# Optimization experiments

Hardware: AMD Instinct MI355X
Metric: run time of the kernel (lower is better)

Reference implementation:

```python
import jax, jax.numpy as jnp
import numpy as np

N_ENTITY = 64368
N_REL = 40
DIM = 128
N_BASES = 8
N_EDGES = 500000
BATCH = 64
SEED_LEN = 32


def _glorot(k, shape, gain=1.414):
    fan_in, fan_out = shape[0], shape[1]
    bound = gain * np.sqrt(6.0 / (fan_in + fan_out))
    return jax.random.uniform(k, shape, jnp.float32, -bound, bound)


def setup_inputs() -> dict:
    key = jax.random.key(0)
    ks = jax.random.split(key, 11)
    return dict(
        seed_ids=jax.random.randint(ks[0], (BATCH, SEED_LEN), 0, N_ENTITY),
        edge_src=jax.random.randint(ks[1], (N_EDGES,), 0, N_ENTITY),
        edge_dst=jax.random.randint(ks[2], (N_EDGES,), 0, N_ENTITY),
        edge_type=jax.random.randint(ks[3], (N_EDGES,), 0, N_REL),
        basis=jax.random.normal(ks[4], (N_BASES, N_ENTITY, DIM), jnp.float32) * 0.02,
        att=jax.random.normal(ks[5], (N_REL, N_BASES), jnp.float32) * 0.1,
        root=jax.random.normal(ks[6], (N_ENTITY, DIM), jnp.float32) * 0.02,
        rgcn_bias=jnp.zeros((DIM,), jnp.float32),
        attn_a=_glorot(ks[7], (DIM, DIM)),
        attn_b=_glorot(ks[8], (DIM, 1)),
        out_bias=jnp.zeros((N_ENTITY,), jnp.float32),
    )


def _rgcn_nodes(basis, att, root, rgcn_bias, edge_src, edge_dst, edge_type):
    # RGCNConv with x=None: message for edge e is row src[e] of w[type[e]],
    # where w = att @ basis (basis decomposition); 'mean' aggregation to dst;
    # update: aggr + root + bias.
    n_entity, dim = root.shape
    coeff = att[edge_type]  # [E, nb]
    agg = jnp.zeros((n_entity, dim), jnp.float32)
    for b in range(basis.shape[0]):  # small fixed loop over bases
        m = basis[b][edge_src] * coeff[:, b][:, None]  # [E, dim]
        agg = agg + jax.ops.segment_sum(m, edge_dst, num_segments=n_entity)
    deg = jax.ops.segment_sum(jnp.ones_like(edge_dst, jnp.float32), edge_dst,
                              num_segments=n_entity)
    agg = agg / jnp.maximum(deg, 1.0)[:, None]
    return agg + root + rgcn_bias[None, :]


def reference(seed_ids, edge_src, edge_dst, edge_type, basis, att, root,
              rgcn_bias, attn_a, attn_b, out_bias):
    nodes = _rgcn_nodes(basis, att, root, rgcn_bias, edge_src, edge_dst, edge_type)
    # self-attention pooling over each seed set (all entries valid / non-empty)
    H = nodes[seed_ids]  # [B, S, D]
    e = jnp.einsum('bsd,d->bs', jnp.tanh(jnp.einsum('bsd,de->bse', H, attn_a)),
                   attn_b[:, 0])  # [B, S]
    attn = jax.nn.softmax(e, axis=-1)
    u = jnp.einsum('bs,bsd->bd', attn, H)  # [B, D]
    # scores = F.linear(u, nodes_features, output.bias)
    scores = u @ nodes.T + out_bias[None, :]  # [B, n_entity]
    return scores
```

## Files before the change

### kernel.cpp

```cpp
#include <hip/hip_runtime.h>
#include <hip/hip_fp16.h>

#define N_ENTITY 64368
#define N_REL 40
#define DIM 128
#define N_BASES 8
#define N_EDGES 500000
#define BATCH 64
#define SEED_LEN 32
#define NROWS (BATCH * SEED_LEN)
#define SCAN_NB ((N_ENTITY + 255) / 256)
#define NPAD (SCAN_NB * 256)

#define CAP 64
#define OVF_CAP 4096
#define SCAT4_BLOCKS ((N_EDGES / 4 + 255) / 256)
#define CVT_BLOCKS 2048


struct alignas(16) h8 { __half2 a, b, c, d; };

__device__ __forceinline__ void scat1(
    int s, int d, int y, int* __restrict__ cnt, int* __restrict__ novf,
    int* __restrict__ ovf, int* __restrict__ slots)
{
    int meta = s * 64 + y;
    int k = atomicAdd(&cnt[d], 1);
    if (k < CAP) {
        slots[(size_t)d * CAP + k] = meta;
    } else {
        int o = atomicAdd(novf, 1);
        if (o < OVF_CAP) { ovf[2 * o] = d; ovf[2 * o + 1] = meta; }
    }
}

__global__ __launch_bounds__(256) void k_prep(
    const int* __restrict__ esrc, const int* __restrict__ edst,
    const int* __restrict__ etype, const float* __restrict__ basis,
    __half* __restrict__ basis16, int* __restrict__ cnt,
    int* __restrict__ novf, int* __restrict__ ovf, int* __restrict__ slots)
{
    int bid = blockIdx.x, tid = threadIdx.x;
    if (bid < SCAT4_BLOCKS) {
        int e4 = (bid * 256 + tid) * 4;
        if (e4 < N_EDGES) {
            int4 s4 = *(const int4*)(esrc + e4);
            int4 d4 = *(const int4*)(edst + e4);
            int4 y4 = *(const int4*)(etype + e4);
            scat1(s4.x, d4.x, y4.x, cnt, novf, ovf, slots);
            scat1(s4.y, d4.y, y4.y, cnt, novf, ovf, slots);
            scat1(s4.z, d4.z, y4.z, cnt, novf, ovf, slots);
            scat1(s4.w, d4.w, y4.w, cnt, novf, ovf, slots);
        }
    } else {
        int lane = tid & 63;
        int l32  = lane & 31;
        int hw   = lane >> 5;
        int wv   = ((bid - SCAT4_BLOCKS) << 2) + (tid >> 6);
        const size_t bstride = (size_t)N_ENTITY * DIM;

        for (int e2 = wv; 2 * e2 < N_ENTITY; e2 += (CVT_BLOCKS << 2)) {
            int e = 2 * e2 + hw;
            if (e >= N_ENTITY) continue;
            const float* sp = basis + (size_t)e * DIM + (l32 << 2);
            __half* dp = basis16 + ((size_t)e << 10) + (l32 << 5);
            #pragma unroll
            for (int it = 0; it < 4; ++it) {
                float4 v0 = *(const float4*)(sp + (size_t)(2 * it)     * bstride);
                float4 v1 = *(const float4*)(sp + (size_t)(2 * it + 1) * bstride);
                h8 o;
                o.a = __floats2half2_rn(v0.x, v0.y);
                o.b = __floats2half2_rn(v0.z, v0.w);
                o.c = __floats2half2_rn(v1.x, v1.y);
                o.d = __floats2half2_rn(v1.z, v1.w);
                *(h8*)(dp + it * 8) = o;
            }
        }
    }
}

__device__ __forceinline__ void acc_edge2(
    const h8& q0, const h8& q1, float4 c, float4& acc)
{
    float2 f;
    f = __half22float2(q0.a); acc.x += c.x * f.x; acc.y += c.x * f.y;
    f = __half22float2(q0.b); acc.z += c.x * f.x; acc.w += c.x * f.y;
    f = __half22float2(q0.c); acc.x += c.y * f.x; acc.y += c.y * f.y;
    f = __half22float2(q0.d); acc.z += c.y * f.x; acc.w += c.y * f.y;
    f = __half22float2(q1.a); acc.x += c.z * f.x; acc.y += c.z * f.y;
    f = __half22float2(q1.b); acc.z += c.z * f.x; acc.w += c.z * f.y;
    f = __half22float2(q1.c); acc.x += c.w * f.x; acc.y += c.w * f.y;
    f = __half22float2(q1.d); acc.z += c.w * f.x; acc.w += c.w * f.y;
}

__global__ __launch_bounds__(256) void k_gather16(
    const int* __restrict__ cnt, const int* __restrict__ novf,
    const int* __restrict__ ovf, const int* __restrict__ slots,
    const __half* __restrict__ basis16, const float* __restrict__ att,
    const float* __restrict__ root, const float* __restrict__ bias,
    float* __restrict__ agg)
{
    __shared__ float att_s[N_REL * N_BASES];
    int tid = threadIdx.x;
    for (int i = tid; i < N_REL * N_BASES; i += 256) att_s[i] = att[i];
    __syncthreads();

    int wid  = (int)((blockIdx.x * 256 + tid) >> 6);
    int lane = tid & 63;
    if (wid >= N_ENTITY) return;
    int par = lane & 1;
    const int loff = lane << 4;

    int c = cnt[wid];
    int n = (c < CAP) ? c : CAP;
    const int* sl = slots + (size_t)wid * CAP;

    float4 acc = {0.f, 0.f, 0.f, 0.f};
    int j = 0;
    for (; j + 3 < n; j += 4) {
        int4 mm = *(const int4*)(sl + j);
        const __half* p0 = basis16 + ((size_t)(mm.x >> 6) << 10) + loff;
        const __half* p1 = basis16 + ((size_t)(mm.y >> 6) << 10) + loff;
        const __half* p2 = basis16 + ((size_t)(mm.z >> 6) << 10) + loff;
        const __half* p3 = basis16 + ((size_t)(mm.w >> 6) << 10) + loff;
        h8 a0 = *(const h8*)(p0);  h8 b0 = *(const h8*)(p0 + 8);
        h8 a1 = *(const h8*)(p1);  h8 b1 = *(const h8*)(p1 + 8);
        h8 a2 = *(const h8*)(p2);  h8 b2 = *(const h8*)(p2 + 8);
        h8 a3 = *(const h8*)(p3);  h8 b3 = *(const h8*)(p3 + 8);
        float4 c0 = *(const float4*)(att_s + (mm.x & 63) * N_BASES + par * 4);
        float4 c1 = *(const float4*)(att_s + (mm.y & 63) * N_BASES + par * 4);
        float4 c2 = *(const float4*)(att_s + (mm.z & 63) * N_BASES + par * 4);
        float4 c3 = *(const float4*)(att_s + (mm.w & 63) * N_BASES + par * 4);
        acc_edge2(a0, b0, c0, acc);
        acc_edge2(a1, b1, c1, acc);
        acc_edge2(a2, b2, c2, acc);
        acc_edge2(a3, b3, c3, acc);
    }
    for (; j < n; ++j) {
        int m = sl[j];
        const __half* p = basis16 + ((size_t)(m >> 6) << 10) + loff;
        h8 q0 = *(const h8*)(p);  h8 q1 = *(const h8*)(p + 8);
        float4 cc = *(const float4*)(att_s + (m & 63) * N_BASES + par * 4);
        acc_edge2(q0, q1, cc, acc);
    }
    if (c > CAP) {
        int nov = *novf; if (nov > OVF_CAP) nov = OVF_CAP;
        for (int k = 0; k < nov; ++k) {
            if (ovf[2 * k] == wid) {
                int m = ovf[2 * k + 1];
                const __half* p = basis16 + ((size_t)(m >> 6) << 10) + loff;
                h8 q0 = *(const h8*)(p);  h8 q1 = *(const h8*)(p + 8);
                float4 cc = *(const float4*)(att_s + (m & 63) * N_BASES + par * 4);
                acc_edge2(q0, q1, cc, acc);
            }
        }
    }

    acc.x += __shfl_xor(acc.x, 1, 64);
    acc.y += __shfl_xor(acc.y, 1, 64);
    acc.z += __shfl_xor(acc.z, 1, 64);
    acc.w += __shfl_xor(acc.w, 1, 64);

    float inv = 1.0f / fmaxf((float)c, 1.0f);
    int dof = ((lane >> 1) << 2) + par * 2;
    int o = wid * DIM + dof;
    float2 r  = *(const float2*)(root + o);
    float2 bb = *(const float2*)(bias + dof);
    float2 outv;
    float vx = par ? acc.z : acc.x;
    float vy = par ? acc.w : acc.y;
    outv.x = vx * inv + r.x + bb.x;
    outv.y = vy * inv + r.y + bb.y;
    *(float2*)(agg + o) = outv;
}

__global__ __launch_bounds__(256) void k_attn(
    const int* __restrict__ seed_ids, const float* __restrict__ nodes,
    const float* __restrict__ A, const float* __restrict__ Bv,
    float* __restrict__ uT)
{
    __shared__ float Hs[SEED_LEN * DIM];
    __shared__ float ew[SEED_LEN];
    __shared__ float attw[SEED_LEN];

    int b = blockIdx.x, tid = threadIdx.x;

    for (int i = tid; i < SEED_LEN * DIM; i += 256) {
        int ss = i >> 7, d = i & 127;
        Hs[i] = nodes[(size_t)seed_ids[b * SEED_LEN + ss] * DIM + d];
    }
    __syncthreads();

    int jx = tid & 31;
    int iy = tid >> 5;
    float acc[4][4] = {{0,0,0,0},{0,0,0,0},{0,0,0,0},{0,0,0,0}};

    for (int d = 0; d < DIM; ++d) {
        const float4 a4 = *(const float4*)(A + d * DIM + jx * 4);
        float h0 = Hs[(iy * 4 + 0) * DIM + d];
        float h1 = Hs[(iy * 4 + 1) * DIM + d];
        float h2 = Hs[(iy * 4 + 2) * DIM + d];
        float h3 = Hs[(iy * 4 + 3) * DIM + d];
        acc[0][0] += h0 * a4.x; acc[0][1] += h0 * a4.y;
        acc[0][2] += h0 * a4.z; acc[0][3] += h0 * a4.w;
        acc[1][0] += h1 * a4.x; acc[1][1] += h1 * a4.y;
        acc[1][2] += h1 * a4.z; acc[1][3] += h1 * a4.w;
        acc[2][0] += h2 * a4.x; acc[2][1] += h2 * a4.y;
        acc[2][2] += h2 * a4.z; acc[2][3] += h2 * a4.w;
        acc[3][0] += h3 * a4.x; acc[3][1] += h3 * a4.y;
        acc[3][2] += h3 * a4.z; acc[3][3] += h3 * a4.w;
    }

    const float4 bv = *(const float4*)(Bv + jx * 4);
    #pragma unroll
    for (int i = 0; i < 4; ++i) {
        float pe = tanhf(acc[i][0]) * bv.x + tanhf(acc[i][1]) * bv.y
                 + tanhf(acc[i][2]) * bv.z + tanhf(acc[i][3]) * bv.w;
        pe += __shfl_xor(pe, 1, 64);
        pe += __shfl_xor(pe, 2, 64);
        pe += __shfl_xor(pe, 4, 64);
        pe += __shfl_xor(pe, 8, 64);
        pe += __shfl_xor(pe, 16, 64);
        if (jx == 0) ew[iy * 4 + i] = pe;
    }
    __syncthreads();

    if (tid == 0) {
        float mx = -1e30f;
        for (int k = 0; k < SEED_LEN; ++k) mx = fmaxf(mx, ew[k]);
        float ssum = 0.0f;
        for (int k = 0; k < SEED_LEN; ++k) {
            float v = expf(ew[k] - mx);
            attw[k] = v; ssum += v;
        }
        float inv = 1.0f / ssum;
        for (int k = 0; k < SEED_LEN; ++k) attw[k] *= inv;
    }
    __syncthreads();

    if (tid < DIM) {
        float a = 0.0f;
        for (int k = 0; k < SEED_LEN; ++k) a += attw[k] * Hs[k * DIM + tid];
        uT[tid * BATCH + b] = a;
    }
}

__global__ __launch_bounds__(256) void k_scores(
    const float* __restrict__ nodes, const float* __restrict__ uT,
    const float* __restrict__ out_bias, float* __restrict__ out)
{
    __shared__ float Nl[DIM * 65];

    int tid = threadIdx.x;
    int n0  = blockIdx.x * 64;

    for (int i = tid; i < 64 * DIM; i += 256) {
        int n = i >> 7, d = i & 127;
        int gn = n0 + n;
        Nl[d * 65 + n] = (gn < N_ENTITY) ? nodes[(size_t)gn * DIM + d] : 0.0f;
    }
    __syncthreads();

    int w    = __builtin_amdgcn_readfirstlane(tid >> 6);
    int lane = tid & 63;
    int b0   = w * 16;

    float acc[16];
    #pragma unroll
    for (int k = 0; k < 16; ++k) acc[k] = 0.0f;

    #pragma unroll 4
    for (int d = 0; d < DIM; ++d) {
        float nv = Nl[d * 65 + lane];
        const float* up = uT + d * BATCH + b0;
        #pragma unroll
        for (int k = 0; k < 16; ++k) acc[k] += up[k] * nv;
    }

    int gn = n0 + lane;
    if (gn < N_ENTITY) {
        float ob = out_bias[gn];
        #pragma unroll
        for (int k = 0; k < 16; ++k)
            out[(size_t)(b0 + k) * N_ENTITY + gn] = acc[k] + ob;
    }
}

__global__ __launch_bounds__(256) void k_histF(
    const int* __restrict__ edst, int* __restrict__ hist)
{
    int e = blockIdx.x * 256 + threadIdx.x;
    if (e < N_EDGES) atomicAdd(&hist[edst[e]], 1);
}

__global__ __launch_bounds__(256) void k_scan1F(
    const int* __restrict__ hist, int* __restrict__ ptr,
    int* __restrict__ partial)
{
    __shared__ int s[256];
    int tid = threadIdx.x;
    int gid = blockIdx.x * 256 + tid;
    int v = hist[gid];
    s[tid] = v;
    __syncthreads();
    for (int off = 1; off < 256; off <<= 1) {
        int t = (tid >= off) ? s[tid - off] : 0;
        __syncthreads();
        s[tid] += t;
        __syncthreads();
    }
    ptr[gid] = s[tid] - v;
    if (tid == 255) partial[blockIdx.x] = s[255];
}

__global__ __launch_bounds__(256) void k_scan23F(
    int* __restrict__ ptr, const int* __restrict__ partial,
    int* __restrict__ work)
{
    __shared__ int s[256];
    int tid = threadIdx.x;
    int c   = blockIdx.x;
    int sum = 0;
    for (int k = tid; k < c; k += 256) sum += partial[k];
    s[tid] = sum;
    __syncthreads();
    for (int off = 128; off > 0; off >>= 1) {
        if (tid < off) s[tid] += s[tid + off];
        __syncthreads();
    }
    int p = ptr[c * 256 + tid] + s[0];
    ptr[c * 256 + tid]  = p;
    work[c * 256 + tid] = p;
}

__global__ __launch_bounds__(256) void k_scatterF(
    const int* __restrict__ esrc, const int* __restrict__ edst,
    const int* __restrict__ etype, int* __restrict__ work,
    int* __restrict__ meta)
{
    int e = blockIdx.x * 256 + threadIdx.x;
    if (e < N_EDGES) {
        int pos = atomicAdd(&work[edst[e]], 1);
        meta[pos] = esrc[e] * 64 + etype[e];
    }
}

#define ACC8(C0, C1, V0, V1, V2, V3, V4, V5, V6, V7)                         \
    acc.x += C0.x*V0.x + C0.y*V1.x + C0.z*V2.x + C0.w*V3.x                   \
           + C1.x*V4.x + C1.y*V5.x + C1.z*V6.x + C1.w*V7.x;                  \
    acc.y += C0.x*V0.y + C0.y*V1.y + C0.z*V2.y + C0.w*V3.y                   \
           + C1.x*V4.y + C1.y*V5.y + C1.z*V6.y + C1.w*V7.y;                  \
    acc.z += C0.x*V0.z + C0.y*V1.z + C0.z*V2.z + C0.w*V3.z                   \
           + C1.x*V4.z + C1.y*V5.z + C1.z*V6.z + C1.w*V7.z;                  \
    acc.w += C0.x*V0.w + C0.y*V1.w + C0.z*V2.w + C0.w*V3.w                   \
           + C1.x*V4.w + C1.y*V5.w + C1.z*V6.w + C1.w*V7.w;

__global__ __launch_bounds__(256) void k_gatherF(
    const int* __restrict__ ptr, const int* __restrict__ hist,
    const int* __restrict__ meta, const float* __restrict__ basis,
    const float* __restrict__ att, const float* __restrict__ root,
    const float* __restrict__ bias, float* __restrict__ agg)
{
    __shared__ float att_s[N_REL * N_BASES];
    int tid = threadIdx.x;
    for (int i = tid; i < N_REL * N_BASES; i += 256) att_s[i] = att[i];
    __syncthreads();

    int wid  = (int)((blockIdx.x * 256 + tid) >> 6);
    int lane = tid & 63;
    if (wid >= N_ENTITY) return;

    int half = lane >> 5;
    int l32  = lane & 31;
    int p   = ptr[wid];
    int cnt = hist[wid];
    const size_t bstride = (size_t)N_ENTITY * DIM;

    float4 acc = {0.f, 0.f, 0.f, 0.f};
    int j = 0;
    for (; j < cnt; j += 2) {
        int m0 = meta[p + j];
        bool has1 = (j + 1 < cnt);
        int m1 = has1 ? meta[p + j + 1] : m0;
        int m = half ? m1 : m0;
        float sc = (half && !has1) ? 0.0f : 1.0f;
        const float* bA = basis + (size_t)(m >> 6) * DIM + l32 * 4;
        float4 a0 = *(const float4*)(bA + 0 * bstride);
        float4 a1 = *(const float4*)(bA + 1 * bstride);
        float4 a2 = *(const float4*)(bA + 2 * bstride);
        float4 a3 = *(const float4*)(bA + 3 * bstride);
        float4 a4 = *(const float4*)(bA + 4 * bstride);
        float4 a5 = *(const float4*)(bA + 5 * bstride);
        float4 a6 = *(const float4*)(bA + 6 * bstride);
        float4 a7 = *(const float4*)(bA + 7 * bstride);
        float4 c0 = *(const float4*)(att_s + (m & 63) * N_BASES);
        float4 c1 = *(const float4*)(att_s + (m & 63) * N_BASES + 4);
        c0.x *= sc; c0.y *= sc; c0.z *= sc; c0.w *= sc;
        c1.x *= sc; c1.y *= sc; c1.z *= sc; c1.w *= sc;
        ACC8(c0, c1, a0, a1, a2, a3, a4, a5, a6, a7)
    }

    acc.x += __shfl_xor(acc.x, 32, 64);
    acc.y += __shfl_xor(acc.y, 32, 64);
    acc.z += __shfl_xor(acc.z, 32, 64);
    acc.w += __shfl_xor(acc.w, 32, 64);

    if (half == 0) {
        float inv = 1.0f / fmaxf((float)cnt, 1.0f);
        int o = wid * DIM + l32 * 4;
        float4 r  = *(const float4*)(root + o);
        float4 bb = *(const float4*)(bias + l32 * 4);
        float4 outv;
        outv.x = acc.x * inv + r.x + bb.x;
        outv.y = acc.y * inv + r.y + bb.y;
        outv.z = acc.z * inv + r.z + bb.z;
        outv.w = acc.w * inv + r.w + bb.w;
        *(float4*)(agg + o) = outv;
    }
}

extern "C" void kernel_launch(void* const* d_in, const int* in_sizes, int n_in,
                              void* d_out, int out_size, void* d_ws, size_t ws_size,
                              hipStream_t stream)
{
    const int*   seed_ids  = (const int*)d_in[0];
    const int*   esrc      = (const int*)d_in[1];
    const int*   edst      = (const int*)d_in[2];
    const int*   etype     = (const int*)d_in[3];
    const float* basis     = (const float*)d_in[4];
    const float* att       = (const float*)d_in[5];
    const float* root      = (const float*)d_in[6];
    const float* rgcn_bias = (const float*)d_in[7];
    const float* attn_a    = (const float*)d_in[8];
    const float* attn_b    = (const float*)d_in[9];
    const float* out_bias  = (const float*)d_in[10];
    float* out = (float*)d_out;

    const size_t AGG_F  = (size_t)N_ENTITY * DIM;
    const size_t B16_W  = (size_t)N_ENTITY * 512;
    const size_t SLOT_W = (size_t)NPAD * CAP;

    const size_t main_words = AGG_F + B16_W + NPAD + 16 + 2 * OVF_CAP
                            + SLOT_W + 2 * BATCH * DIM + 64;
    bool big = ws_size >= main_words * 4;

    if (big) {
        float*  agg     = (float*)d_ws;
        __half* basis16 = (__half*)(agg + AGG_F);
        int*    cnt     = (int*)(agg + AGG_F + B16_W);
        int*    novf    = cnt + NPAD;
        int*    ovf     = novf + 16;
        int*    slots   = ovf + 2 * OVF_CAP;
        float*  uT      = (float*)(slots + SLOT_W);

        hipMemsetAsync(cnt, 0, (NPAD + 16) * sizeof(int), stream);
        k_prep<<<SCAT4_BLOCKS + CVT_BLOCKS, 256, 0, stream>>>(
            esrc, edst, etype, basis, basis16, cnt, novf, ovf, slots);
        k_gather16<<<(N_ENTITY * 64 + 255) / 256, 256, 0, stream>>>(
            cnt, novf, ovf, slots, basis16, att, root, rgcn_bias, agg);
        k_attn<<<BATCH, 256, 0, stream>>>(seed_ids, agg, attn_a, attn_b, uT);
        k_scores<<<(N_ENTITY + 63) / 64, 256, 0, stream>>>(agg, uT, out_bias, out);
    } else {
        float* agg   = (float*)d_ws;
        int*   hist  = (int*)(agg + AGG_F);
        int*   ptr   = hist + NPAD;
        int*   work  = ptr + NPAD;
        int*   part  = work + NPAD;
        int*   meta  = part + 256;
        float* uT    = (float*)(meta + N_EDGES);

        hipMemsetAsync(hist, 0, NPAD * sizeof(int), stream);
        k_histF<<<(N_EDGES + 255) / 256, 256, 0, stream>>>(edst, hist);
        k_scan1F<<<SCAN_NB, 256, 0, stream>>>(hist, ptr, part);
        k_scan23F<<<SCAN_NB, 256, 0, stream>>>(ptr, part, work);
        k_scatterF<<<(N_EDGES + 255) / 256, 256, 0, stream>>>(
            esrc, edst, etype, work, meta);
        k_gatherF<<<(N_ENTITY * 64 + 255) / 256, 256, 0, stream>>>(
            ptr, hist, meta, basis, att, root, rgcn_bias, agg);
        k_attn<<<BATCH, 256, 0, stream>>>(seed_ids, agg, attn_a, attn_b, uT);
        k_scores<<<(N_ENTITY + 63) / 64, 256, 0, stream>>>(agg, uT, out_bias, out);
    }
}
```

Baseline: 638.8 us.

## Compute per-edge messages source-major from fp32 basis, then reduce per destination

Replaces the fp16 basis conversion and destination-side gather with a two-phase scheme. Edges are bucketed by both source and destination. Phase A has each source row load its 8 basis rows once and compute the att-weighted message for every outgoing edge, writing fp16 messages into destination slots. Phase B then sums contiguous messages per destination. This removes the full basis-to-fp16 conversion pass and the random 2KB gathers per edge, in exchange for a 500k x 128 fp16 message buffer write plus read and two atomic counters per edge. Overflow edges fall back to slow per-thread scalar loops or float atomics on agg.

```diff
diff --git a/kernel.cpp b/kernel.cpp
--- a/kernel.cpp
+++ b/kernel.cpp
@@ -12,165 +12,190 @@
 #define SCAN_NB ((N_ENTITY + 255) / 256)
 #define NPAD (SCAN_NB * 256)
 
-#define CAP 64
-#define OVF_CAP 4096
-#define SCAT4_BLOCKS ((N_EDGES / 4 + 255) / 256)
-#define CVT_BLOCKS 2048
-
-
-struct alignas(16) h8 { __half2 a, b, c, d; };
-
-__device__ __forceinline__ void scat1(
-    int s, int d, int y, int* __restrict__ cnt, int* __restrict__ novf,
-    int* __restrict__ ovf, int* __restrict__ slots)
-{
-    int meta = s * 64 + y;
-    int k = atomicAdd(&cnt[d], 1);
-    if (k < CAP) {
-        slots[(size_t)d * CAP + k] = meta;
-    } else {
-        int o = atomicAdd(novf, 1);
-        if (o < OVF_CAP) { ovf[2 * o] = d; ovf[2 * o + 1] = meta; }
-    }
-}
-
-__global__ __launch_bounds__(256) void k_prep(
+#define CAP_S 40
+#define CAP_D 40
+
+struct alignas(8) half4 { __half2 lo, hi; };
+
+__global__ __launch_bounds__(256) void k_scatter(
     const int* __restrict__ esrc, const int* __restrict__ edst,
     const int* __restrict__ etype, const float* __restrict__ basis,
-    __half* __restrict__ basis16, int* __restrict__ cnt,
-    int* __restrict__ novf, int* __restrict__ ovf, int* __restrict__ slots)
-{
-    int bid = blockIdx.x, tid = threadIdx.x;
-    if (bid < SCAT4_BLOCKS) {
-        int e4 = (bid * 256 + tid) * 4;
-        if (e4 < N_EDGES) {
-            int4 s4 = *(const int4*)(esrc + e4);
-            int4 d4 = *(const int4*)(edst + e4);
-            int4 y4 = *(const int4*)(etype + e4);
-            scat1(s4.x, d4.x, y4.x, cnt, novf, ovf, slots);
-            scat1(s4.y, d4.y, y4.y, cnt, novf, ovf, slots);
-            scat1(s4.z, d4.z, y4.z, cnt, novf, ovf, slots);
-            scat1(s4.w, d4.w, y4.w, cnt, novf, ovf, slots);
+    const float* __restrict__ att, int* __restrict__ cnts,
+    int* __restrict__ cntd, int* __restrict__ slots,
+    __half* __restrict__ msg, float* __restrict__ agg)
+{
+    int e = blockIdx.x * 256 + threadIdx.x;
+    if (e >= N_EDGES) return;
+    int s = esrc[e], d = edst[e], t = etype[e];
+
+    int kd = atomicAdd(&cntd[d], 1);
+    unsigned pack;
+    if (kd < CAP_D) pack = ((unsigned)(d * CAP_D + kd) << 6) | (unsigned)t;
+    else            pack = 0x80000000u | ((unsigned)d << 6) | (unsigned)t;
+
+    int ks = atomicAdd(&cnts[s], 1);
+    if (ks < CAP_S) {
+        slots[(size_t)s * CAP_S + ks] = (int)pack;
+    } else {
+        const size_t bstride = (size_t)N_ENTITY * DIM;
+        for (int dd = 0; dd < DIM; ++dd) {
+            float m = 0.f;
+            #pragma unroll
+            for (int b = 0; b < N_BASES; ++b)
+                m += att[t * N_BASES + b] * basis[b * bstride + (size_t)s * DIM + dd];
+            if (kd < CAP_D)
+                msg[(size_t)(d * CAP_D + kd) * DIM + dd] = __float2half(m);
+            else
+                unsafeAtomicAdd(&agg[(size_t)d * DIM + dd], m);
         }
-    } else {
-        int lane = tid & 63;
-        int l32  = lane & 31;
-        int hw   = lane >> 5;
-        int wv   = ((bid - SCAT4_BLOCKS) << 2) + (tid >> 6);
-        const size_t bstride = (size_t)N_ENTITY * DIM;
-
-        for (int e2 = wv; 2 * e2 < N_ENTITY; e2 += (CVT_BLOCKS << 2)) {
-            int e = 2 * e2 + hw;
-            if (e >= N_ENTITY) continue;
-            const float* sp = basis + (size_t)e * DIM + (l32 << 2);
-            __half* dp = basis16 + ((size_t)e << 10) + (l32 << 5);
-            #pragma unroll
-            for (int it = 0; it < 4; ++it) {
-                float4 v0 = *(const float4*)(sp + (size_t)(2 * it)     * bstride);
-                float4 v1 = *(const float4*)(sp + (size_t)(2 * it + 1) * bstride);
-                h8 o;
-                o.a = __floats2half2_rn(v0.x, v0.y);
-                o.b = __floats2half2_rn(v0.z, v0.w);
-                o.c = __floats2half2_rn(v1.x, v1.y);
-                o.d = __floats2half2_rn(v1.z, v1.w);
-                *(h8*)(dp + it * 8) = o;
-            }
-        }
-    }
-}
-
-__device__ __forceinline__ void acc_edge2(
-    const h8& q0, const h8& q1, float4 c, float4& acc)
-{
-    float2 f;
-    f = __half22float2(q0.a); acc.x += c.x * f.x; acc.y += c.x * f.y;
-    f = __half22float2(q0.b); acc.z += c.x * f.x; acc.w += c.x * f.y;
-    f = __half22float2(q0.c); acc.x += c.y * f.x; acc.y += c.y * f.y;
-    f = __half22float2(q0.d); acc.z += c.y * f.x; acc.w += c.y * f.y;
-    f = __half22float2(q1.a); acc.x += c.z * f.x; acc.y += c.z * f.y;
-    f = __half22float2(q1.b); acc.z += c.z * f.x; acc.w += c.z * f.y;
-    f = __half22float2(q1.c); acc.x += c.w * f.x; acc.y += c.w * f.y;
-    f = __half22float2(q1.d); acc.z += c.w * f.x; acc.w += c.w * f.y;
-}
-
-__global__ __launch_bounds__(256) void k_gather16(
-    const int* __restrict__ cnt, const int* __restrict__ novf,
-    const int* __restrict__ ovf, const int* __restrict__ slots,
-    const __half* __restrict__ basis16, const float* __restrict__ att,
-    const float* __restrict__ root, const float* __restrict__ bias,
-    float* __restrict__ agg)
+    }
+}
+
+__global__ __launch_bounds__(256) void k_phaseA(
+    const int* __restrict__ cnts, const int* __restrict__ slots,
+    const float* __restrict__ basis, const float* __restrict__ att,
+    __half* __restrict__ msg, float* __restrict__ agg)
 {
     __shared__ float att_s[N_REL * N_BASES];
     int tid = threadIdx.x;
     for (int i = tid; i < N_REL * N_BASES; i += 256) att_s[i] = att[i];
     __syncthreads();
 
-    int wid  = (int)((blockIdx.x * 256 + tid) >> 6);
-    int lane = tid & 63;
+    int sid = (blockIdx.x * 256 + tid) >> 5;
+    int l32 = tid & 31;
+    if (sid >= N_ENTITY) return;
+    int cnt = cnts[sid];
+    if (cnt == 0) return;
+    if (cnt > CAP_S) cnt = CAP_S;
+    const int* sl = slots + (size_t)sid * CAP_S;
+
+    const size_t bstride = (size_t)N_ENTITY * DIM;
+    const float* bp = basis + (size_t)sid * DIM + l32 * 4;
+    float4 r0 = *(const float4*)(bp + 0 * bstride);
+    float4 r1 = *(const float4*)(bp + 1 * bstride);
+    float4 r2 = *(const float4*)(bp + 2 * bstride);
+    float4 r3 = *(const float4*)(bp + 3 * bstride);
+    float4 r4 = *(const float4*)(bp + 4 * bstride);
+    float4 r5 = *(const float4*)(bp + 5 * bstride);
+    float4 r6 = *(const float4*)(bp + 6 * bstride);
+    float4 r7 = *(const float4*)(bp + 7 * bstride);
+
+    int j = 0;
+    for (; j + 1 < cnt; j += 2) {
+        int pA = sl[j];
+        int pB = sl[j + 1];
+        const float* cAp = att_s + (pA & 63) * N_BASES;
+        const float* cBp = att_s + (pB & 63) * N_BASES;
+        float4 cA0 = *(const float4*)(cAp);
+        float4 cA1 = *(const float4*)(cAp + 4);
+        float4 cB0 = *(const float4*)(cBp);
+        float4 cB1 = *(const float4*)(cBp + 4);
+
+        float4 mA, mB;
+        mA.x = cA0.x*r0.x + cA0.y*r1.x + cA0.z*r2.x + cA0.w*r3.x
+             + cA1.x*r4.x + cA1.y*r5.x + cA1.z*r6.x + cA1.w*r7.x;
+        mA.y = cA0.x*r0.y + cA0.y*r1.y + cA0.z*r2.y + cA0.w*r3.y
+             + cA1.x*r4.y + cA1.y*r5.y + cA1.z*r6.y + cA1.w*r7.y;
+        mA.z = cA0.x*r0.z + cA0.y*r1.z + cA0.z*r2.z + cA0.w*r3.z
+             + cA1.x*r4.z + cA1.y*r5.z + cA1.z*r6.z + cA1.w*r7.z;
+        mA.w = cA0.x*r0.w + cA0.y*r1.w + cA0.z*r2.w + cA0.w*r3.w
+             + cA1.x*r4.w + cA1.y*r5.w + cA1.z*r6.w + cA1.w*r7.w;
+        mB.x = cB0.x*r0.x + cB0.y*r1.x + cB0.z*r2.x + cB0.w*r3.x
+             + cB1.x*r4.x + cB1.y*r5.x + cB1.z*r6.x + cB1.w*r7.x;
+        mB.y = cB0.x*r0.y + cB0.y*r1.y + cB0.z*r2.y + cB0.w*r3.y
+             + cB1.x*r4.y + cB1.y*r5.y + cB1.z*r6.y + cB1.w*r7.y;
+        mB.z = cB0.x*r0.z + cB0.y*r1.z + cB0.z*r2.z + cB0.w*r3.z
+             + cB1.x*r4.z + cB1.y*r5.z + cB1.z*r6.z + cB1.w*r7.z;
+        mB.w = cB0.x*r0.w + cB0.y*r1.w + cB0.z*r2.w + cB0.w*r3.w
+             + cB1.x*r4.w + cB1.y*r5.w + cB1.z*r6.w + cB1.w*r7.w;
+
+        half4 hA, hB;
+        hA.lo = __floats2half2_rn(mA.x, mA.y);
+        hA.hi = __floats2half2_rn(mA.z, mA.w);
+        hB.lo = __floats2half2_rn(mB.x, mB.y);
+        hB.hi = __floats2half2_rn(mB.z, mB.w);
+        if (pA >= 0) {
+            *(half4*)(msg + ((size_t)((unsigned)pA >> 6) << 7) + (l32 << 2)) = hA;
+        } else {
+            int dd = (int)(((unsigned)pA >> 6) & 0x1FFFFu);
+            float* ap = agg + (size_t)dd * DIM + l32 * 4;
+            unsafeAtomicAdd(ap + 0, mA.x); unsafeAtomicAdd(ap + 1, mA.y);
+            unsafeAtomicAdd(ap + 2, mA.z); unsafeAtomicAdd(ap + 3, mA.w);
+        }
+        if (pB >= 0) {
+            *(half4*)(msg + ((size_t)((unsigned)pB >> 6) << 7) + (l32 << 2)) = hB;
+        } else {
+            int dd = (int)(((unsigned)pB >> 6) & 0x1FFFFu);
+            float* ap = agg + (size_t)dd * DIM + l32 * 4;
+            unsafeAtomicAdd(ap + 0, mB.x); unsafeAtomicAdd(ap + 1, mB.y);
+            unsafeAtomicAdd(ap + 2, mB.z); unsafeAtomicAdd(ap + 3, mB.w);
+        }
+    }
+    if (j < cnt) {
+        int pA = sl[j];
+        const float* cAp = att_s + (pA & 63) * N_BASES;
+        float4 cA0 = *(const float4*)(cAp);
+        float4 cA1 = *(const float4*)(cAp + 4);
+        float4 mA;
+        mA.x = cA0.x*r0.x + cA0.y*r1.x + cA0.z*r2.x + cA0.w*r3.x
+             + cA1.x*r4.x + cA1.y*r5.x + cA1.z*r6.x + cA1.w*r7.x;
+        mA.y = cA0.x*r0.y + cA0.y*r1.y + cA0.z*r2.y + cA0.w*r3.y
+             + cA1.x*r4.y + cA1.y*r5.y + cA1.z*r6.y + cA1.w*r7.y;
+        mA.z = cA0.x*r0.z + cA0.y*r1.z + cA0.z*r2.z + cA0.w*r3.z
+             + cA1.x*r4.z + cA1.y*r5.z + cA1.z*r6.z + cA1.w*r7.z;
+        mA.w = cA0.x*r0.w + cA0.y*r1.w + cA0.z*r2.w + cA0.w*r3.w
+             + cA1.x*r4.w + cA1.y*r5.w + cA1.z*r6.w + cA1.w*r7.w;
+        half4 hA;
+        hA.lo = __floats2half2_rn(mA.x, mA.y);
+        hA.hi = __floats2half2_rn(mA.z, mA.w);
+        if (pA >= 0) {
+            *(half4*)(msg + ((size_t)((unsigned)pA >> 6) << 7) + (l32 << 2)) = hA;
+        } else {
+            int dd = (int)(((unsigned)pA >> 6) & 0x1FFFFu);
+            float* ap = agg + (size_t)dd * DIM + l32 * 4;
+            unsafeAtomicAdd(ap + 0, mA.x); unsafeAtomicAdd(ap + 1, mA.y);
+            unsafeAtomicAdd(ap + 2, mA.z); unsafeAtomicAdd(ap + 3, mA.w);
+        }
+    }
+}
+
+__global__ __launch_bounds__(256) void k_phaseB(
+    const int* __restrict__ cntd, const __half* __restrict__ msg,
+    const float* __restrict__ root, const float* __restrict__ bias,
+    float* __restrict__ agg)
+{
+    int wid  = (int)((blockIdx.x * 256 + threadIdx.x) >> 6);
+    int lane = threadIdx.x & 63;
     if (wid >= N_ENTITY) return;
-    int par = lane & 1;
-    const int loff = lane << 4;
-
-    int c = cnt[wid];
-    int n = (c < CAP) ? c : CAP;
-    const int* sl = slots + (size_t)wid * CAP;
-
-    float4 acc = {0.f, 0.f, 0.f, 0.f};
+    int c = cntd[wid];
+    int n = (c < CAP_D) ? c : CAP_D;
+    const __half2* mp = (const __half2*)msg + (size_t)wid * (CAP_D * 64) + lane;
+
+    float ax = 0.f, ay = 0.f;
     int j = 0;
     for (; j + 3 < n; j += 4) {
-        int4 mm = *(const int4*)(sl + j);
-        const __half* p0 = basis16 + ((size_t)(mm.x >> 6) << 10) + loff;
-        const __half* p1 = basis16 + ((size_t)(mm.y >> 6) << 10) + loff;
-        const __half* p2 = basis16 + ((size_t)(mm.z >> 6) << 10) + loff;
-        const __half* p3 = basis16 + ((size_t)(mm.w >> 6) << 10) + loff;
-        h8 a0 = *(const h8*)(p0);  h8 b0 = *(const h8*)(p0 + 8);
-        h8 a1 = *(const h8*)(p1);  h8 b1 = *(const h8*)(p1 + 8);
-        h8 a2 = *(const h8*)(p2);  h8 b2 = *(const h8*)(p2 + 8);
-        h8 a3 = *(const h8*)(p3);  h8 b3 = *(const h8*)(p3 + 8);
-        float4 c0 = *(const float4*)(att_s + (mm.x & 63) * N_BASES + par * 4);
-        float4 c1 = *(const float4*)(att_s + (mm.y & 63) * N_BASES + par * 4);
-        float4 c2 = *(const float4*)(att_s + (mm.z & 63) * N_BASES + par * 4);
-        float4 c3 = *(const float4*)(att_s + (mm.w & 63) * N_BASES + par * 4);
-        acc_edge2(a0, b0, c0, acc);
-        acc_edge2(a1, b1, c1, acc);
-        acc_edge2(a2, b2, c2, acc);
-        acc_edge2(a3, b3, c3, acc);
+        float2 f0 = __half22float2(mp[(j + 0) * 64]);
+        float2 f1 = __half22float2(mp[(j + 1) * 64]);
+        float2 f2 = __half22float2(mp[(j + 2) * 64]);
+        float2 f3 = __half22float2(mp[(j + 3) * 64]);
+        ax += (f0.x + f1.x) + (f2.x + f3.x);
+        ay += (f0.y + f1.y) + (f2.y + f3.y);
     }
     for (; j < n; ++j) {
-        int m = sl[j];
-        const __half* p = basis16 + ((size_t)(m >> 6) << 10) + loff;
-        h8 q0 = *(const h8*)(p);  h8 q1 = *(const h8*)(p + 8);
-        float4 cc = *(const float4*)(att_s + (m & 63) * N_BASES + par * 4);
-        acc_edge2(q0, q1, cc, acc);
-    }
-    if (c > CAP) {
-        int nov = *novf; if (nov > OVF_CAP) nov = OVF_CAP;
-        for (int k = 0; k < nov; ++k) {
-            if (ovf[2 * k] == wid) {
-                int m = ovf[2 * k + 1];
-                const __half* p = basis16 + ((size_t)(m >> 6) << 10) + loff;
-                h8 q0 = *(const h8*)(p);  h8 q1 = *(const h8*)(p + 8);
-                float4 cc = *(const float4*)(att_s + (m & 63) * N_BASES + par * 4);
-                acc_edge2(q0, q1, cc, acc);
-            }
-        }
-    }
-
-    acc.x += __shfl_xor(acc.x, 1, 64);
-    acc.y += __shfl_xor(acc.y, 1, 64);
-    acc.z += __shfl_xor(acc.z, 1, 64);
-    acc.w += __shfl_xor(acc.w, 1, 64);
+        float2 f = __half22float2(mp[j * 64]);
+        ax += f.x; ay += f.y;
+    }
+
+    int o = wid * DIM + lane * 2;
+    float2 prev = *(const float2*)(agg + o);
+    ax += prev.x; ay += prev.y;
 
     float inv = 1.0f / fmaxf((float)c, 1.0f);
-    int dof = ((lane >> 1) << 2) + par * 2;
-    int o = wid * DIM + dof;
     float2 r  = *(const float2*)(root + o);
-    float2 bb = *(const float2*)(bias + dof);
+    float2 bb = *(const float2*)(bias + lane * 2);
     float2 outv;
-    float vx = par ? acc.z : acc.x;
-    float vy = par ? acc.w : acc.y;
-    outv.x = vx * inv + r.x + bb.x;
-    outv.y = vy * inv + r.y + bb.y;
+    outv.x = ax * inv + r.x + bb.x;
+    outv.y = ay * inv + r.y + bb.y;
     *(float2*)(agg + o) = outv;
 }
 
@@ -436,28 +461,30 @@
     const float* out_bias  = (const float*)d_in[10];
     float* out = (float*)d_out;
 
-    const size_t AGG_F  = (size_t)N_ENTITY * DIM;
-    const size_t B16_W  = (size_t)N_ENTITY * 512;
-    const size_t SLOT_W = (size_t)NPAD * CAP;
-
-    const size_t main_words = AGG_F + B16_W + NPAD + 16 + 2 * OVF_CAP
-                            + SLOT_W + 2 * BATCH * DIM + 64;
+    const size_t AGG_F   = (size_t)N_ENTITY * DIM;
+    const size_t SLOTS_W = (size_t)N_ENTITY * CAP_S;
+    const size_t MSG_W   = (size_t)N_ENTITY * CAP_D * DIM / 2;
+
+    const size_t main_words = AGG_F + 2 * NPAD + SLOTS_W + MSG_W
+                            + 2 * BATCH * DIM + 64;
     bool big = ws_size >= main_words * 4;
 
     if (big) {
-        float*  agg     = (float*)d_ws;
-        __half* basis16 = (__half*)(agg + AGG_F);
-        int*    cnt     = (int*)(agg + AGG_F + B16_W);
-        int*    novf    = cnt + NPAD;
-        int*    ovf     = novf + 16;
-        int*    slots   = ovf + 2 * OVF_CAP;
-        float*  uT      = (float*)(slots + SLOT_W);
-
-        hipMemsetAsync(cnt, 0, (NPAD + 16) * sizeof(int), stream);
-        k_prep<<<SCAT4_BLOCKS + CVT_BLOCKS, 256, 0, stream>>>(
-            esrc, edst, etype, basis, basis16, cnt, novf, ovf, slots);
-        k_gather16<<<(N_ENTITY * 64 + 255) / 256, 256, 0, stream>>>(
-            cnt, novf, ovf, slots, basis16, att, root, rgcn_bias, agg);
+        float*  agg   = (float*)d_ws;
+        int*    cntd  = (int*)(agg + AGG_F);
+        int*    cnts  = cntd + NPAD;
+        int*    slots = cnts + NPAD;
+        __half* msg   = (__half*)(slots + SLOTS_W);
+        float*  uT    = (float*)((int*)msg + MSG_W);
+
+        hipMemsetAsync(d_ws, 0, (AGG_F + 2 * NPAD) * sizeof(int), stream);
+
+        k_scatter<<<(N_EDGES + 255) / 256, 256, 0, stream>>>(
+            esrc, edst, etype, basis, att, cnts, cntd, slots, msg, agg);
+        k_phaseA<<<N_ENTITY / 8, 256, 0, stream>>>(
+            cnts, slots, basis, att, msg, agg);
+        k_phaseB<<<(N_ENTITY + 3) / 4, 256, 0, stream>>>(
+            cntd, msg, root, rgcn_bias, agg);
         k_attn<<<BATCH, 256, 0, stream>>>(seed_ids, agg, attn_a, attn_b, uT);
         k_scores<<<(N_ENTITY + 63) / 64, 256, 0, stream>>>(agg, uT, out_bias, out);
     } else {
```

Result: faster. 569.0 us (-10.9%).
